# Kernel optimization log

Measured on AMD Instinct MI355X. Metric: run time of the kernel, lower is better.

The kernel has to match this reference:

```python
import jax, jax.numpy as jnp
import numpy as np

C = 256
CK = C // 8  # query/key projection dim

def conv1x1(x, w, b):
    # x: (B,C,H,W), w: (O,C), b: (O,)
    return jnp.einsum('bchw,oc->bohw', x, w) + b[None, :, None, None]

def conv3x3(x, w, b):
    # w: (O,C,3,3)
    y = jax.lax.conv_general_dilated(x, w, window_strides=(1, 1), padding='SAME',
                                     dimension_numbers=('NCHW', 'OIHW', 'NCHW'))
    return y + b[None, :, None, None]

def setup_inputs() -> dict:
    key = jax.random.key(0)
    ks = jax.random.split(key, 24)
    s = 0.05
    d = {
        'x1': jax.random.normal(ks[0], (4, C, 64, 64), jnp.float32),
        'x2': jax.random.normal(ks[1], (4, C, 64, 64), jnp.float32),
        'wq1': jax.random.normal(ks[2], (CK, C), jnp.float32) * s,
        'bq1': jax.random.normal(ks[3], (CK,), jnp.float32) * s,
        'wk1': jax.random.normal(ks[4], (CK, C), jnp.float32) * s,
        'bk1': jax.random.normal(ks[5], (CK,), jnp.float32) * s,
        'wv1': jax.random.normal(ks[6], (C, C), jnp.float32) * s,
        'bv1': jax.random.normal(ks[7], (C,), jnp.float32) * s,
        'wq2': jax.random.normal(ks[8], (CK, C), jnp.float32) * s,
        'bq2': jax.random.normal(ks[9], (CK,), jnp.float32) * s,
        'wk2': jax.random.normal(ks[10], (CK, C), jnp.float32) * s,
        'bk2': jax.random.normal(ks[11], (CK,), jnp.float32) * s,
        'wv2': jax.random.normal(ks[12], (C, C), jnp.float32) * s,
        'bv2': jax.random.normal(ks[13], (C,), jnp.float32) * s,
        'wd1': jax.random.normal(ks[14], (C, C), jnp.float32) * s,
        'bd1': jax.random.normal(ks[15], (C,), jnp.float32) * s,
        'wd3': jax.random.normal(ks[16], (C, C, 3, 3), jnp.float32) * s,
        'bd3': jax.random.normal(ks[17], (C,), jnp.float32) * s,
        'gamma1': jax.random.normal(ks[18], (1,), jnp.float32) * 0.5,
        'gamma2': jax.random.normal(ks[19], (1,), jnp.float32) * 0.5,
    }
    return d

def reference(x1, x2, wq1, bq1, wk1, bk1, wv1, bv1, wq2, bq2, wk2, bk2, wv2, bv2,
              wd1, bd1, wd3, bd3, gamma1, gamma2):
    B, Cc, H, W = x1.shape
    N = H * W
    # projections (1x1 convs), flattened to (B, d, N)
    q1 = conv1x1(x1, wq1, bq1).reshape(B, CK, N)
    k1 = conv1x1(x1, wk1, bk1).reshape(B, CK, N)
    v1 = conv1x1(x1, wv1, bv1).reshape(B, Cc, N)
    q2 = conv1x1(x2, wq2, bq2).reshape(B, CK, N)
    k2 = conv1x1(x2, wk2, bk2).reshape(B, CK, N)
    v2 = conv1x1(x2, wv2, bv2).reshape(B, Cc, N)
    # cross attention 1: queries from x1, keys/values from x2
    energy1 = jnp.einsum('bdi,bdj->bij', q1, k2)          # (B,N,N)
    attn1 = jax.nn.softmax(energy1, axis=-1)
    out1 = jnp.einsum('bcj,bij->bci', v2, attn1).reshape(B, Cc, H, W)
    # cross attention 2: queries from x2, keys/values from x1
    energy2 = jnp.einsum('bdi,bdj->bij', q2, k1)
    attn2 = jax.nn.softmax(energy2, axis=-1)
    out2 = jnp.einsum('bcj,bij->bci', v1, attn2).reshape(B, Cc, H, W)
    # residual conv branches + gamma-scaled skip (norm1/norm2 in source are dead code)
    out1 = out1 + conv1x1(x1, wd1, bd1) + conv3x3(x1, wd3, bd3)
    out2 = out2 + conv1x1(x2, wd1, bd1) + conv3x3(x2, wd3, bd3)
    out1 = x1 + gamma1[0] * out1
    out2 = x2 + gamma2[0] * out2
    return (out1, out2)
```

## Files before the change

kernel.cpp:

```cpp
#include <hip/hip_runtime.h>
#include <hip/hip_bf16.h>

#define CC 256
#define CKD 32
#define NN 4096
#define HH 64
#define WW 64
#define BB 4

#define LOG2E 1.44269504088896f
#define EXPSHIFT 23.0831203874f

typedef __attribute__((ext_vector_type(8))) short short8;
typedef __attribute__((ext_vector_type(4))) float floatx4;

__device__ __forceinline__ unsigned f2bf(float f) {
  union { float f; unsigned u; } v; v.f = f;
  unsigned r = v.u + 0x7fffu + ((v.u >> 16) & 1u);
  return r >> 16;
}
__device__ __forceinline__ unsigned f2bf_fast(float f) {
  return (__float_as_uint(f) + 0x8000u) >> 16;
}
__device__ __forceinline__ float fast_exp2(float x) {
#if __has_builtin(__builtin_amdgcn_exp2f)
  return __builtin_amdgcn_exp2f(x);
#else
  return __expf(x * 0.693147181f);
#endif
}
__device__ __forceinline__ float bf_lo(unsigned u) { return __uint_as_float(u << 16); }
__device__ __forceinline__ float bf_hi(unsigned u) { return __uint_as_float(u & 0xffff0000u); }

__device__ __forceinline__ void bar_lds() {
  asm volatile("s_waitcnt lgkmcnt(0)" ::: "memory");
  __builtin_amdgcn_s_barrier();
}

__global__ __launch_bounds__(256) void xpack_kernel(
    const float* __restrict__ x1, const float* __restrict__ x2,
    unsigned short* __restrict__ Xp) {
  const int t = threadIdx.x;
  const int nb = blockIdx.x, cbk = blockIdx.y, img = blockIdx.z;
  const float* X = ((img >> 2) ? x2 : x1) + (size_t)(img & 3) * CC * NN;
  const int n0 = nb * 64, c0 = cbk * 64;
  __shared__ float tile[64][65];
  const int nl = t & 63, cl0 = t >> 6;
#pragma unroll
  for (int i = 0; i < 16; ++i)
    tile[cl0 + i * 4][nl] = X[(size_t)(c0 + cl0 + i * 4) * NN + n0 + nl];
  __syncthreads();
#pragma unroll
  for (int it = 0; it < 2; ++it) {
    int id = it * 256 + t;
    int nl2 = id >> 3, cc = id & 7;
    short8 v;
#pragma unroll
    for (int j = 0; j < 8; ++j) v[j] = (short)f2bf(tile[cc * 8 + j][nl2]);
    *(short8*)(Xp + (size_t)img * NN * CC + (size_t)(n0 + nl2) * CC + c0 + cc * 8) = v;
  }
}

__global__ __launch_bounds__(256) void wpack_kernel(
    const float* __restrict__ wd1, const float* __restrict__ wd3,
    const float* __restrict__ wq1, const float* __restrict__ wk1,
    const float* __restrict__ wv1,
    const float* __restrict__ wq2, const float* __restrict__ wk2,
    const float* __restrict__ wv2,
    const float* __restrict__ bq1, const float* __restrict__ bk1,
    const float* __restrict__ bv1,
    const float* __restrict__ bq2, const float* __restrict__ bk2,
    const float* __restrict__ bv2,
    unsigned short* __restrict__ Wp, unsigned short* __restrict__ Wqkv,
    float* __restrict__ Bias) {
  const int id = blockIdx.x * 256 + threadIdx.x;
#pragma unroll
  for (int tap = 0; tap < 10; ++tap) {
    float v = (tap < 9) ? wd3[(size_t)id * 9 + tap] : wd1[id];
    Wp[(size_t)tap * (CC * CC) + id] = (unsigned short)f2bf(v);
  }
#pragma unroll
  for (int j = 0; j < 3; ++j) {
    int e = id + j * 65536;
    if (e < 2 * 320 * 256) {
      int inp = e / (320 * 256), rem = e % (320 * 256);
      int o = rem >> 8, c = rem & 255;
      float v;
      if (inp == 0)
        v = (o < 32) ? wq1[o * 256 + c] * LOG2E
            : (o < 64) ? wk1[(o - 32) * 256 + c] : wv1[(o - 64) * 256 + c];
      else
        v = (o < 32) ? wq2[o * 256 + c] * LOG2E
            : (o < 64) ? wk2[(o - 32) * 256 + c] : wv2[(o - 64) * 256 + c];
      Wqkv[e] = (unsigned short)f2bf(v);
    }
  }
  if (id < 640) {
    int inp = id / 320, o = id % 320;
    float v;
    if (inp == 0) v = (o < 32) ? bq1[o] * LOG2E
                      : (o < 64) ? bk1[o - 32] : bv1[o - 64];
    else          v = (o < 32) ? bq2[o] * LOG2E
                      : (o < 64) ? bk2[o - 32] : bv2[o - 64];
    Bias[id] = v;
  }
}

__global__ __launch_bounds__(256) void proj_mfma_kernel(
    const unsigned short* __restrict__ Xp, const unsigned short* __restrict__ Wqkv,
    const float* __restrict__ Bias,
    unsigned short* __restrict__ Qp1, unsigned short* __restrict__ Kp1,
    unsigned short* __restrict__ Vp1,
    unsigned short* __restrict__ Qp2, unsigned short* __restrict__ Kp2,
    unsigned short* __restrict__ Vp2) {
  const int t = threadIdx.x;
  const int w = t >> 6, lane = t & 63;
  const int l15 = lane & 15, g = lane >> 4;
  const int img = blockIdx.x, pb = blockIdx.y;
  const int pix0 = pb * 64;
  const int inp = img >> 2, b = img & 3;
  const unsigned short* Xi = Xp + (size_t)img * NN * CC;
  const unsigned short* Wb = Wqkv + (size_t)inp * 320 * CC;
  const float* Bi = Bias + inp * 320;
  unsigned short* Qp = (inp ? Qp2 : Qp1) + (size_t)b * NN * CKD;
  unsigned short* Kp = (inp ? Kp2 : Kp1) + (size_t)b * NN * CKD;
  unsigned short* Vp = (inp ? Vp2 : Vp1) + (size_t)b * NN * CC;

  __shared__ unsigned short tile[320][72];

  floatx4 acc[4][5];
#pragma unroll
  for (int mf = 0; mf < 4; ++mf)
#pragma unroll
    for (int nf = 0; nf < 5; ++nf) acc[mf][nf] = (floatx4){0.f, 0.f, 0.f, 0.f};
  const int o0w = w * 80;

#pragma unroll
  for (int cb = 0; cb < 8; ++cb) {
    short8 a[4], bfr[5];
#pragma unroll
    for (int mf = 0; mf < 4; ++mf)
      a[mf] = *(const short8*)(Xi + (size_t)(pix0 + mf * 16 + l15) * CC + cb * 32 + g * 8);
#pragma unroll
    for (int nf = 0; nf < 5; ++nf)
      bfr[nf] = *(const short8*)(Wb + (size_t)(o0w + nf * 16 + l15) * CC + cb * 32 + g * 8);
#pragma unroll
    for (int nf = 0; nf < 5; ++nf)
#pragma unroll
      for (int mf = 0; mf < 4; ++mf)
        acc[mf][nf] = __builtin_amdgcn_mfma_f32_16x16x32_bf16(
            a[mf], bfr[nf], acc[mf][nf], 0, 0, 0);
  }

#pragma unroll
  for (int nf = 0; nf < 5; ++nf) {
    float bs = Bi[o0w + nf * 16 + l15];
#pragma unroll
    for (int mf = 0; mf < 4; ++mf) {
      uint2 pk;
      pk.x = f2bf(acc[mf][nf][0] + bs) | (f2bf(acc[mf][nf][1] + bs) << 16);
      pk.y = f2bf(acc[mf][nf][2] + bs) | (f2bf(acc[mf][nf][3] + bs) << 16);
      *(uint2*)&tile[o0w + nf * 16 + l15][mf * 16 + g * 4] = pk;
    }
  }
  __syncthreads();

  {
    const int pix = t >> 2, ch = t & 3;
    short8 vq, vk;
#pragma unroll
    for (int e = 0; e < 8; ++e) {
      vq[e] = (short)tile[ch * 8 + e][pix];
      vk[e] = (short)tile[32 + ch * 8 + e][pix];
    }
    *(short8*)(Qp + (size_t)(pix0 + pix) * CKD + ch * 8) = vq;
    *(short8*)(Kp + (size_t)(pix0 + pix) * CKD + ch * 8) = vk;
  }
#pragma unroll
  for (int it = 0; it < 8; ++it) {
    short8 vv = *(const short8*)&tile[64 + t][it * 8];
    *(short8*)(Vp + ((size_t)((pix0 >> 3) + it) * CC + t) * 8) = vv;
  }
}

__global__ __launch_bounds__(256, 2) void attn_kernel(
    const unsigned short* __restrict__ Qp1, const unsigned short* __restrict__ Kp1,
    const unsigned short* __restrict__ Qp2, const unsigned short* __restrict__ Kp2,
    const unsigned short* __restrict__ Vp1, const unsigned short* __restrict__ Vp2,
    const unsigned short* __restrict__ Xp, const unsigned short* __restrict__ Wp,
    const float* __restrict__ bd1, const float* __restrict__ bd3,
    const float* __restrict__ x1, const float* __restrict__ x2,
    const float* __restrict__ g1, const float* __restrict__ g2,
    float* __restrict__ out) {
  const int t = threadIdx.x;
  const int w = t >> 6, lane = t & 63;
  const int l15 = lane & 15, g = lane >> 4;
  const int att = blockIdx.x, b = blockIdx.y;
  const int yblk = blockIdx.z;
  const int i0 = yblk * 64;

  const unsigned short *Qp, *Kp, *Vp; const float *x; float gamma; float* o;
  if (att == 0) { Qp = Qp1; Kp = Kp2; Vp = Vp2; x = x1; gamma = g1[0]; o = out; }
  else          { Qp = Qp2; Kp = Kp1; Vp = Vp1; x = x2; gamma = g2[0];
                  o = out + (size_t)BB * CC * NN; }
  Qp += (size_t)b * NN * CKD; Kp += (size_t)b * NN * CKD; Vp += (size_t)b * NN * CC;
  x += (size_t)b * CC * NN; o += (size_t)b * CC * NN;
  const unsigned short* Xi = Xp + (size_t)(att * 4 + b) * NN * CC;

  __shared__ union {
    unsigned short xs[3][66][72];
    unsigned short ps[2][64][72];
  } u;
  __shared__ unsigned short cres[256][68];
  __shared__ float l_s[64];

  short8 bq = *(const short8*)(Qp + (size_t)(i0 + w * 16 + l15) * CKD + g * 8);

  floatx4 acc[4][4];
#pragma unroll
  for (int a = 0; a < 4; ++a)
#pragma unroll
    for (int c = 0; c < 4; ++c) acc[a][c] = (floatx4){0.f, 0.f, 0.f, 0.f};
  float l_acc = 0.f;
  const floatx4 zinit = {-EXPSHIFT, -EXPSHIFT, -EXPSHIFT, -EXPSHIFT};

  short8 kr[2][4], vr[2][8];
  auto LOADK = [&](int tt, short8* d) {
    const unsigned short* kb = Kp + ((size_t)tt * 64 + l15) * CKD + g * 8;
#pragma unroll
    for (int js = 0; js < 4; ++js) d[js] = *(const short8*)(kb + js * 16 * CKD);
  };
  auto LOADV = [&](int tt, short8* d) {
#pragma unroll
    for (int ks = 0; ks < 2; ++ks)
#pragma unroll
      for (int cs = 0; cs < 4; ++cs)
        d[ks * 4 + cs] = *(const short8*)(Vp +
            (((size_t)tt * 8 + ks * 4 + g) * CC + (w * 64 + cs * 16 + l15)) * 8);
  };
  auto GEMM1 = [&](const short8* kb, unsigned short (*ps)[72]) {
#pragma unroll
    for (int js = 0; js < 4; ++js) {
      floatx4 s = __builtin_amdgcn_mfma_f32_16x16x32_bf16(kb[js], bq, zinit, 0, 0, 0);
      float p0 = fast_exp2(s[0]);
      float p1 = fast_exp2(s[1]);
      float p2 = fast_exp2(s[2]);
      float p3 = fast_exp2(s[3]);
      l_acc += (p0 + p1) + (p2 + p3);
      unsigned u0 = __float_as_uint(p0) + 0x8000u;
      unsigned u1 = __float_as_uint(p1) + 0x8000u;
      unsigned u2 = __float_as_uint(p2) + 0x8000u;
      unsigned u3 = __float_as_uint(p3) + 0x8000u;
      uint2 pk;
      pk.x = __builtin_amdgcn_perm(u1, u0, 0x07060302u);
      pk.y = __builtin_amdgcn_perm(u3, u2, 0x07060302u);
      *(uint2*)&ps[w * 16 + l15][js * 16 + g * 4] = pk;
    }
  };
  auto GEMM2 = [&](const short8* vb, unsigned short (*ps)[72]) {
#pragma unroll
    for (int ks = 0; ks < 2; ++ks) {
      short8 ap[4];
#pragma unroll
      for (int isub = 0; isub < 4; ++isub)
        ap[isub] = *(const short8*)&ps[isub * 16 + l15][ks * 32 + g * 8];
#pragma unroll
      for (int cs = 0; cs < 4; ++cs)
#pragma unroll
        for (int isub = 0; isub < 4; ++isub)
          acc[isub][cs] = __builtin_amdgcn_mfma_f32_16x16x32_bf16(
              ap[isub], vb[ks * 4 + cs], acc[isub][cs], 0, 0, 0);
    }
  };

  LOADK(0, kr[0]); LOADK(1, kr[1]); LOADV(0, vr[0]);

  {
    floatx4 ac[4][4];
#pragma unroll
    for (int pm = 0; pm < 4; ++pm)
#pragma unroll
      for (int on = 0; on < 4; ++on) ac[pm][on] = (floatx4){0.f, 0.f, 0.f, 0.f};

    for (int cb = 0; cb < 4; ++cb) {
      const int c0 = cb * 64;
      if (cb) bar_lds();
#pragma unroll
      for (int it = 0; it < 7; ++it) {
        int id = it * 256 + t;
        if (id < 1584) {
          int r = id / 528, rem = id % 528;
          int col = rem >> 3, cc = rem & 7;
          int y = yblk - 1 + r, xx = col - 1;
          short8 v = {0, 0, 0, 0, 0, 0, 0, 0};
          if (y >= 0 && y < HH && xx >= 0 && xx < WW)
            v = *(const short8*)(Xi + (size_t)(y * WW + xx) * CC + c0 + cc * 8);
          *(short8*)&u.xs[r][col][cc * 8] = v;
        }
      }
      bar_lds();
#pragma unroll
      for (int tap = 0; tap < 10; ++tap) {
        const int dy = (tap < 9) ? tap / 3 - 1 : 0;
        const int dx = (tap < 9) ? tap % 3 - 1 : 0;
        const unsigned short* wrow =
            Wp + ((size_t)tap * CC + w * 64 + l15) * CC + c0 + g * 8;
#pragma unroll
        for (int ks = 0; ks < 2; ++ks) {
          short8 af[4], bw[4];
#pragma unroll
          for (int pm = 0; pm < 4; ++pm)
            af[pm] = *(const short8*)&u.xs[1 + dy][1 + pm * 16 + l15 + dx][ks * 32 + g * 8];
#pragma unroll
          for (int on = 0; on < 4; ++on)
            bw[on] = *(const short8*)(wrow + (size_t)(on * 16) * CC + ks * 32);
#pragma unroll
          for (int pm = 0; pm < 4; ++pm)
#pragma unroll
            for (int on = 0; on < 4; ++on)
              ac[pm][on] = __builtin_amdgcn_mfma_f32_16x16x32_bf16(
                  af[pm], bw[on], ac[pm][on], 0, 0, 0);
        }
      }
    }
#pragma unroll
    for (int on = 0; on < 4; ++on) {
      int oo = w * 64 + on * 16 + l15;
      float bs = bd1[oo] + bd3[oo];
#pragma unroll
      for (int pm = 0; pm < 4; ++pm) {
        uint2 pk;
        pk.x = f2bf_fast(ac[pm][on][0] + bs) | (f2bf_fast(ac[pm][on][1] + bs) << 16);
        pk.y = f2bf_fast(ac[pm][on][2] + bs) | (f2bf_fast(ac[pm][on][3] + bs) << 16);
        *(uint2*)&cres[oo][pm * 16 + g * 4] = pk;
      }
    }
  }
  bar_lds();

  GEMM1(kr[0], u.ps[0]);
  bar_lds();

  for (int jt = 0; jt < 64; jt += 2) {
    if (jt + 2 < 64) LOADK(jt + 2, kr[0]);
    LOADV(jt + 1, vr[1]);
    GEMM1(kr[1], u.ps[1]);
    GEMM2(vr[0], u.ps[0]);
    bar_lds();
    if (jt + 3 < 64) LOADK(jt + 3, kr[1]);
    if (jt + 2 < 64) { LOADV(jt + 2, vr[0]); GEMM1(kr[0], u.ps[0]); }
    GEMM2(vr[1], u.ps[1]);
    bar_lds();
  }

  l_acc += __shfl_xor(l_acc, 16);
  l_acc += __shfl_xor(l_acc, 32);
  if (g == 0) l_s[w * 16 + l15] = l_acc;
  bar_lds();

#pragma unroll
  for (int isub = 0; isub < 4; ++isub) {
    float linv[4];
#pragma unroll
    for (int r = 0; r < 4; ++r) linv[r] = 1.f / l_s[isub * 16 + g * 4 + r];
#pragma unroll
    for (int cs = 0; cs < 4; ++cs) {
      int c = w * 64 + cs * 16 + l15;
      size_t base = (size_t)c * NN + i0 + isub * 16 + g * 4;
      float4 xr = *(const float4*)(x + base);
      uint2 cr = *(const uint2*)&cres[c][isub * 16 + g * 4];
      float4 ov;
      ov.x = xr.x + gamma * (acc[isub][cs][0] * linv[0] + bf_lo(cr.x));
      ov.y = xr.y + gamma * (acc[isub][cs][1] * linv[1] + bf_hi(cr.x));
      ov.z = xr.z + gamma * (acc[isub][cs][2] * linv[2] + bf_lo(cr.y));
      ov.w = xr.w + gamma * (acc[isub][cs][3] * linv[3] + bf_hi(cr.y));
      *(float4*)(o + base) = ov;
    }
  }
}

extern "C" void kernel_launch(void* const* d_in, const int* in_sizes, int n_in,
                              void* d_out, int out_size, void* d_ws, size_t ws_size,
                              hipStream_t stream) {
  const float* x1  = (const float*)d_in[0];
  const float* x2  = (const float*)d_in[1];
  const float* wq1 = (const float*)d_in[2];
  const float* bq1 = (const float*)d_in[3];
  const float* wk1 = (const float*)d_in[4];
  const float* bk1 = (const float*)d_in[5];
  const float* wv1 = (const float*)d_in[6];
  const float* bv1 = (const float*)d_in[7];
  const float* wq2 = (const float*)d_in[8];
  const float* bq2 = (const float*)d_in[9];
  const float* wk2 = (const float*)d_in[10];
  const float* bk2 = (const float*)d_in[11];
  const float* wv2 = (const float*)d_in[12];
  const float* bv2 = (const float*)d_in[13];
  const float* wd1 = (const float*)d_in[14];
  const float* bd1 = (const float*)d_in[15];
  const float* wd3 = (const float*)d_in[16];
  const float* bd3 = (const float*)d_in[17];
  const float* g1  = (const float*)d_in[18];
  const float* g2  = (const float*)d_in[19];
  float* out = (float*)d_out;

  const size_t QB = (size_t)BB * NN * CKD * 2;
  const size_t VB = (size_t)BB * NN * CC * 2;
  const size_t XB = (size_t)2 * BB * NN * CC * 2;
  const size_t WPB = (size_t)10 * CC * CC * 2;
  const size_t WQB = (size_t)2 * 320 * CC * 2;
  char* base = (char*)d_ws;
  unsigned short* Qp1 = (unsigned short*)(base);
  unsigned short* Kp1 = (unsigned short*)(base + QB);
  unsigned short* Qp2 = (unsigned short*)(base + 2 * QB);
  unsigned short* Kp2 = (unsigned short*)(base + 3 * QB);
  unsigned short* Vp1 = (unsigned short*)(base + 4 * QB);
  unsigned short* Vp2 = (unsigned short*)(base + 4 * QB + VB);
  unsigned short* Xp  = (unsigned short*)(base + 4 * QB + 2 * VB);
  unsigned short* Wp  = (unsigned short*)(base + 4 * QB + 2 * VB + XB);
  unsigned short* Wqkv = (unsigned short*)(base + 4 * QB + 2 * VB + XB + WPB);
  float* Bias = (float*)(base + 4 * QB + 2 * VB + XB + WPB + WQB);

  xpack_kernel<<<dim3(NN / 64, CC / 64, 2 * BB), 256, 0, stream>>>(x1, x2, Xp);
  wpack_kernel<<<dim3(CC * CC / 256), 256, 0, stream>>>(
      wd1, wd3, wq1, wk1, wv1, wq2, wk2, wv2,
      bq1, bk1, bv1, bq2, bk2, bv2, Wp, Wqkv, Bias);

  proj_mfma_kernel<<<dim3(2 * BB, NN / 64), 256, 0, stream>>>(
      Xp, Wqkv, Bias, Qp1, Kp1, Vp1, Qp2, Kp2, Vp2);

  attn_kernel<<<dim3(2, BB, NN / 64), 256, 0, stream>>>(
      Qp1, Kp1, Qp2, Kp2, Vp1, Vp2, Xp, Wp, bd1, bd3, x1, x2, g1, g2, out);
}
```

Measured before the change: 302.1 us.

## Load conv3x3 input tiles directly from global memory and raise occupancy to 3 blocks

Removes the LDS staging of the 3-row input halo for the fused 3x3/1x1 conv. Each MFMA operand fragment is now read straight from global memory with bounds-checked zero padding, which also removes the per-channel-block barriers. The smaller LDS footprint (no union, narrower cres padding) plus launch_bounds 3 are meant to fit more blocks per CU. In exchange there are many redundant, uncoalesced global loads that rely on L1/L2 hits, register pressure is tighter, and the cres row stride of 66 may cause LDS bank conflicts.

```diff
diff --git a/kernel.cpp b/kernel.cpp
--- a/kernel.cpp
+++ b/kernel.cpp
@@ -183,7 +183,7 @@
   }
 }
 
-__global__ __launch_bounds__(256, 2) void attn_kernel(
+__global__ __launch_bounds__(256, 3) void attn_kernel(
     const unsigned short* __restrict__ Qp1, const unsigned short* __restrict__ Kp1,
     const unsigned short* __restrict__ Qp2, const unsigned short* __restrict__ Kp2,
     const unsigned short* __restrict__ Vp1, const unsigned short* __restrict__ Vp2,
@@ -207,11 +207,8 @@
   x += (size_t)b * CC * NN; o += (size_t)b * CC * NN;
   const unsigned short* Xi = Xp + (size_t)(att * 4 + b) * NN * CC;
 
-  __shared__ union {
-    unsigned short xs[3][66][72];
-    unsigned short ps[2][64][72];
-  } u;
-  __shared__ unsigned short cres[256][68];
+  __shared__ unsigned short ps[2][64][72];
+  __shared__ unsigned short cres[256][66];
   __shared__ float l_s[64];
 
   short8 bq = *(const short8*)(Qp + (size_t)(i0 + w * 16 + l15) * CKD + g * 8);
@@ -238,7 +235,7 @@
         d[ks * 4 + cs] = *(const short8*)(Vp +
             (((size_t)tt * 8 + ks * 4 + g) * CC + (w * 64 + cs * 16 + l15)) * 8);
   };
-  auto GEMM1 = [&](const short8* kb, unsigned short (*ps)[72]) {
+  auto GEMM1 = [&](const short8* kb, unsigned short (*psb)[72]) {
 #pragma unroll
     for (int js = 0; js < 4; ++js) {
       floatx4 s = __builtin_amdgcn_mfma_f32_16x16x32_bf16(kb[js], bq, zinit, 0, 0, 0);
@@ -254,16 +251,16 @@
       uint2 pk;
       pk.x = __builtin_amdgcn_perm(u1, u0, 0x07060302u);
       pk.y = __builtin_amdgcn_perm(u3, u2, 0x07060302u);
-      *(uint2*)&ps[w * 16 + l15][js * 16 + g * 4] = pk;
+      *(uint2*)&psb[w * 16 + l15][js * 16 + g * 4] = pk;
     }
   };
-  auto GEMM2 = [&](const short8* vb, unsigned short (*ps)[72]) {
+  auto GEMM2 = [&](const short8* vb, unsigned short (*psb)[72]) {
 #pragma unroll
     for (int ks = 0; ks < 2; ++ks) {
       short8 ap[4];
 #pragma unroll
       for (int isub = 0; isub < 4; ++isub)
-        ap[isub] = *(const short8*)&ps[isub * 16 + l15][ks * 32 + g * 8];
+        ap[isub] = *(const short8*)&psb[isub * 16 + l15][ks * 32 + g * 8];
 #pragma unroll
       for (int cs = 0; cs < 4; ++cs)
 #pragma unroll
@@ -284,33 +281,24 @@
 
     for (int cb = 0; cb < 4; ++cb) {
       const int c0 = cb * 64;
-      if (cb) bar_lds();
-#pragma unroll
-      for (int it = 0; it < 7; ++it) {
-        int id = it * 256 + t;
-        if (id < 1584) {
-          int r = id / 528, rem = id % 528;
-          int col = rem >> 3, cc = rem & 7;
-          int y = yblk - 1 + r, xx = col - 1;
-          short8 v = {0, 0, 0, 0, 0, 0, 0, 0};
-          if (y >= 0 && y < HH && xx >= 0 && xx < WW)
-            v = *(const short8*)(Xi + (size_t)(y * WW + xx) * CC + c0 + cc * 8);
-          *(short8*)&u.xs[r][col][cc * 8] = v;
-        }
-      }
-      bar_lds();
 #pragma unroll
       for (int tap = 0; tap < 10; ++tap) {
         const int dy = (tap < 9) ? tap / 3 - 1 : 0;
         const int dx = (tap < 9) ? tap % 3 - 1 : 0;
+        const int y = yblk + dy;
         const unsigned short* wrow =
             Wp + ((size_t)tap * CC + w * 64 + l15) * CC + c0 + g * 8;
 #pragma unroll
         for (int ks = 0; ks < 2; ++ks) {
           short8 af[4], bw[4];
 #pragma unroll
-          for (int pm = 0; pm < 4; ++pm)
-            af[pm] = *(const short8*)&u.xs[1 + dy][1 + pm * 16 + l15 + dx][ks * 32 + g * 8];
+          for (int pm = 0; pm < 4; ++pm) {
+            const int px = pm * 16 + l15 + dx;
+            short8 v = {0, 0, 0, 0, 0, 0, 0, 0};
+            if (((unsigned)y < (unsigned)HH) & ((unsigned)px < (unsigned)WW))
+              v = *(const short8*)(Xi + (size_t)(y * WW + px) * CC + c0 + ks * 32 + g * 8);
+            af[pm] = v;
+          }
 #pragma unroll
           for (int on = 0; on < 4; ++on)
             bw[on] = *(const short8*)(wrow + (size_t)(on * 16) * CC + ks * 32);
@@ -336,20 +324,19 @@
       }
     }
   }
-  bar_lds();
-
-  GEMM1(kr[0], u.ps[0]);
+
+  GEMM1(kr[0], ps[0]);
   bar_lds();
 
   for (int jt = 0; jt < 64; jt += 2) {
     if (jt + 2 < 64) LOADK(jt + 2, kr[0]);
     LOADV(jt + 1, vr[1]);
-    GEMM1(kr[1], u.ps[1]);
-    GEMM2(vr[0], u.ps[0]);
+    GEMM1(kr[1], ps[1]);
+    GEMM2(vr[0], ps[0]);
     bar_lds();
     if (jt + 3 < 64) LOADK(jt + 3, kr[1]);
-    if (jt + 2 < 64) { LOADV(jt + 2, vr[0]); GEMM1(kr[0], u.ps[0]); }
-    GEMM2(vr[1], u.ps[1]);
+    if (jt + 2 < 64) { LOADV(jt + 2, vr[0]); GEMM1(kr[0], ps[0]); }
+    GEMM2(vr[1], ps[1]);
     bar_lds();
   }
 
```

Result: slower. 527.7 us (+74.6%).

## Split attention blocks across channel halves and fold conv into attention accumulators

Applied to the files above, without the earlier changes.

The attention kernel now launches twice as many blocks, each handling half of the output channels. Each warp covers 32 query rows by 64 channels, which halves the accumulator registers and lets occupancy rise to 4 blocks per CU. The residual conv is now computed after attention, accumulating straight into the normalized attention accumulators, so the bf16 cres LDS buffer and its rounding go away. The cost is that GEMM1 (QK^T plus exp) is computed twice, once in each channel-half block, and the K/V pipeline is reworked to single-step double buffering.

```diff
diff --git a/kernel.cpp b/kernel.cpp
--- a/kernel.cpp
+++ b/kernel.cpp
@@ -18,9 +18,6 @@
   union { float f; unsigned u; } v; v.f = f;
   unsigned r = v.u + 0x7fffu + ((v.u >> 16) & 1u);
   return r >> 16;
-}
-__device__ __forceinline__ unsigned f2bf_fast(float f) {
-  return (__float_as_uint(f) + 0x8000u) >> 16;
 }
 __device__ __forceinline__ float fast_exp2(float x) {
 #if __has_builtin(__builtin_amdgcn_exp2f)
@@ -183,7 +180,7 @@
   }
 }
 
-__global__ __launch_bounds__(256, 2) void attn_kernel(
+__global__ __launch_bounds__(256, 4) void attn_kernel(
     const unsigned short* __restrict__ Qp1, const unsigned short* __restrict__ Kp1,
     const unsigned short* __restrict__ Qp2, const unsigned short* __restrict__ Kp2,
     const unsigned short* __restrict__ Vp1, const unsigned short* __restrict__ Vp2,
@@ -195,9 +192,12 @@
   const int t = threadIdx.x;
   const int w = t >> 6, lane = t & 63;
   const int l15 = lane & 15, g = lane >> 4;
-  const int att = blockIdx.x, b = blockIdx.y;
+  const int att = blockIdx.x >> 1, chh = blockIdx.x & 1;
+  const int b = blockIdx.y;
   const int yblk = blockIdx.z;
   const int i0 = yblk * 64;
+  const int ip = w & 1, cq = w >> 1;
+  const int ch0 = chh * 128 + cq * 64;
 
   const unsigned short *Qp, *Kp, *Vp; const float *x; float gamma; float* o;
   if (att == 0) { Qp = Qp1; Kp = Kp2; Vp = Vp2; x = x1; gamma = g1[0]; o = out; }
@@ -208,40 +208,37 @@
   const unsigned short* Xi = Xp + (size_t)(att * 4 + b) * NN * CC;
 
   __shared__ union {
+    unsigned short ps[2][64][72];
     unsigned short xs[3][66][72];
-    unsigned short ps[2][64][72];
   } u;
-  __shared__ unsigned short cres[256][68];
   __shared__ float l_s[64];
 
   short8 bq = *(const short8*)(Qp + (size_t)(i0 + w * 16 + l15) * CKD + g * 8);
 
-  floatx4 acc[4][4];
-#pragma unroll
-  for (int a = 0; a < 4; ++a)
-#pragma unroll
-    for (int c = 0; c < 4; ++c) acc[a][c] = (floatx4){0.f, 0.f, 0.f, 0.f};
+  floatx4 acc[2][4];
+#pragma unroll
+  for (int is = 0; is < 2; ++is)
+#pragma unroll
+    for (int c = 0; c < 4; ++c) acc[is][c] = (floatx4){0.f, 0.f, 0.f, 0.f};
   float l_acc = 0.f;
   const floatx4 zinit = {-EXPSHIFT, -EXPSHIFT, -EXPSHIFT, -EXPSHIFT};
 
-  short8 kr[2][4], vr[2][8];
-  auto LOADK = [&](int tt, short8* d) {
+  short8 kr[4], vA[4], vB[4];
+  auto LOADK = [&](int tt) {
     const unsigned short* kb = Kp + ((size_t)tt * 64 + l15) * CKD + g * 8;
 #pragma unroll
-    for (int js = 0; js < 4; ++js) d[js] = *(const short8*)(kb + js * 16 * CKD);
+    for (int js = 0; js < 4; ++js) kr[js] = *(const short8*)(kb + js * 16 * CKD);
   };
-  auto LOADV = [&](int tt, short8* d) {
-#pragma unroll
-    for (int ks = 0; ks < 2; ++ks)
-#pragma unroll
-      for (int cs = 0; cs < 4; ++cs)
-        d[ks * 4 + cs] = *(const short8*)(Vp +
-            (((size_t)tt * 8 + ks * 4 + g) * CC + (w * 64 + cs * 16 + l15)) * 8);
+  auto LOADVH = [&](int tt, int ks, short8* d) {
+#pragma unroll
+    for (int cs = 0; cs < 4; ++cs)
+      d[cs] = *(const short8*)(Vp +
+          (((size_t)tt * 8 + ks * 4 + g) * CC + (ch0 + cs * 16 + l15)) * 8);
   };
-  auto GEMM1 = [&](const short8* kb, unsigned short (*ps)[72]) {
+  auto GEMM1 = [&](unsigned short (*psb)[72]) {
 #pragma unroll
     for (int js = 0; js < 4; ++js) {
-      floatx4 s = __builtin_amdgcn_mfma_f32_16x16x32_bf16(kb[js], bq, zinit, 0, 0, 0);
+      floatx4 s = __builtin_amdgcn_mfma_f32_16x16x32_bf16(kr[js], bq, zinit, 0, 0, 0);
       float p0 = fast_exp2(s[0]);
       float p1 = fast_exp2(s[1]);
       float p2 = fast_exp2(s[2]);
@@ -254,104 +251,40 @@
       uint2 pk;
       pk.x = __builtin_amdgcn_perm(u1, u0, 0x07060302u);
       pk.y = __builtin_amdgcn_perm(u3, u2, 0x07060302u);
-      *(uint2*)&ps[w * 16 + l15][js * 16 + g * 4] = pk;
+      *(uint2*)&psb[w * 16 + l15][js * 16 + g * 4] = pk;
     }
   };
-  auto GEMM2 = [&](const short8* vb, unsigned short (*ps)[72]) {
-#pragma unroll
-    for (int ks = 0; ks < 2; ++ks) {
-      short8 ap[4];
-#pragma unroll
-      for (int isub = 0; isub < 4; ++isub)
-        ap[isub] = *(const short8*)&ps[isub * 16 + l15][ks * 32 + g * 8];
-#pragma unroll
-      for (int cs = 0; cs < 4; ++cs)
-#pragma unroll
-        for (int isub = 0; isub < 4; ++isub)
-          acc[isub][cs] = __builtin_amdgcn_mfma_f32_16x16x32_bf16(
-              ap[isub], vb[ks * 4 + cs], acc[isub][cs], 0, 0, 0);
-    }
+  auto GEMM2ks = [&](int ks, const short8* vb, unsigned short (*psb)[72]) {
+    short8 ap[2];
+#pragma unroll
+    for (int is = 0; is < 2; ++is)
+      ap[is] = *(const short8*)&psb[(ip * 2 + is) * 16 + l15][ks * 32 + g * 8];
+#pragma unroll
+    for (int cs = 0; cs < 4; ++cs)
+#pragma unroll
+      for (int is = 0; is < 2; ++is)
+        acc[is][cs] = __builtin_amdgcn_mfma_f32_16x16x32_bf16(
+            ap[is], vb[cs], acc[is][cs], 0, 0, 0);
   };
 
-  LOADK(0, kr[0]); LOADK(1, kr[1]); LOADV(0, vr[0]);
-
-  {
-    floatx4 ac[4][4];
-#pragma unroll
-    for (int pm = 0; pm < 4; ++pm)
-#pragma unroll
-      for (int on = 0; on < 4; ++on) ac[pm][on] = (floatx4){0.f, 0.f, 0.f, 0.f};
-
-    for (int cb = 0; cb < 4; ++cb) {
-      const int c0 = cb * 64;
-      if (cb) bar_lds();
-#pragma unroll
-      for (int it = 0; it < 7; ++it) {
-        int id = it * 256 + t;
-        if (id < 1584) {
-          int r = id / 528, rem = id % 528;
-          int col = rem >> 3, cc = rem & 7;
-          int y = yblk - 1 + r, xx = col - 1;
-          short8 v = {0, 0, 0, 0, 0, 0, 0, 0};
-          if (y >= 0 && y < HH && xx >= 0 && xx < WW)
-            v = *(const short8*)(Xi + (size_t)(y * WW + xx) * CC + c0 + cc * 8);
-          *(short8*)&u.xs[r][col][cc * 8] = v;
-        }
-      }
-      bar_lds();
-#pragma unroll
-      for (int tap = 0; tap < 10; ++tap) {
-        const int dy = (tap < 9) ? tap / 3 - 1 : 0;
-        const int dx = (tap < 9) ? tap % 3 - 1 : 0;
-        const unsigned short* wrow =
-            Wp + ((size_t)tap * CC + w * 64 + l15) * CC + c0 + g * 8;
-#pragma unroll
-        for (int ks = 0; ks < 2; ++ks) {
-          short8 af[4], bw[4];
-#pragma unroll
-          for (int pm = 0; pm < 4; ++pm)
-            af[pm] = *(const short8*)&u.xs[1 + dy][1 + pm * 16 + l15 + dx][ks * 32 + g * 8];
-#pragma unroll
-          for (int on = 0; on < 4; ++on)
-            bw[on] = *(const short8*)(wrow + (size_t)(on * 16) * CC + ks * 32);
-#pragma unroll
-          for (int pm = 0; pm < 4; ++pm)
-#pragma unroll
-            for (int on = 0; on < 4; ++on)
-              ac[pm][on] = __builtin_amdgcn_mfma_f32_16x16x32_bf16(
-                  af[pm], bw[on], ac[pm][on], 0, 0, 0);
-        }
-      }
-    }
-#pragma unroll
-    for (int on = 0; on < 4; ++on) {
-      int oo = w * 64 + on * 16 + l15;
-      float bs = bd1[oo] + bd3[oo];
-#pragma unroll
-      for (int pm = 0; pm < 4; ++pm) {
-        uint2 pk;
-        pk.x = f2bf_fast(ac[pm][on][0] + bs) | (f2bf_fast(ac[pm][on][1] + bs) << 16);
-        pk.y = f2bf_fast(ac[pm][on][2] + bs) | (f2bf_fast(ac[pm][on][3] + bs) << 16);
-        *(uint2*)&cres[oo][pm * 16 + g * 4] = pk;
-      }
-    }
-  }
+  LOADK(0); LOADVH(0, 0, vA); LOADVH(0, 1, vB);
+  GEMM1(u.ps[0]);
+  LOADK(1);
   bar_lds();
 
-  GEMM1(kr[0], u.ps[0]);
-  bar_lds();
-
-  for (int jt = 0; jt < 64; jt += 2) {
-    if (jt + 2 < 64) LOADK(jt + 2, kr[0]);
-    LOADV(jt + 1, vr[1]);
-    GEMM1(kr[1], u.ps[1]);
-    GEMM2(vr[0], u.ps[0]);
+  for (int jt = 0; jt < 63; ++jt) {
+    unsigned short (*pcur)[72] = u.ps[jt & 1];
+    unsigned short (*pnxt)[72] = u.ps[(jt & 1) ^ 1];
+    GEMM1(pnxt);
+    if (jt < 62) LOADK(jt + 2);
+    GEMM2ks(0, vA, pcur);
+    LOADVH(jt + 1, 0, vA);
+    GEMM2ks(1, vB, pcur);
+    LOADVH(jt + 1, 1, vB);
     bar_lds();
-    if (jt + 3 < 64) LOADK(jt + 3, kr[1]);
-    if (jt + 2 < 64) { LOADV(jt + 2, vr[0]); GEMM1(kr[0], u.ps[0]); }
-    GEMM2(vr[1], u.ps[1]);
-    bar_lds();
-  }
+  }
+  GEMM2ks(0, vA, u.ps[1]);
+  GEMM2ks(1, vB, u.ps[1]);
 
   l_acc += __shfl_xor(l_acc, 16);
   l_acc += __shfl_xor(l_acc, 32);
@@ -359,21 +292,73 @@
   bar_lds();
 
 #pragma unroll
-  for (int isub = 0; isub < 4; ++isub) {
+  for (int is = 0; is < 2; ++is) {
     float linv[4];
 #pragma unroll
-    for (int r = 0; r < 4; ++r) linv[r] = 1.f / l_s[isub * 16 + g * 4 + r];
+    for (int r = 0; r < 4; ++r)
+      linv[r] = 1.f / l_s[ip * 32 + is * 16 + g * 4 + r];
+#pragma unroll
+    for (int cs = 0; cs < 4; ++cs)
+#pragma unroll
+      for (int r = 0; r < 4; ++r) acc[is][cs][r] *= linv[r];
+  }
+
+  for (int cb = 0; cb < 4; ++cb) {
+    const int c0 = cb * 64;
+    bar_lds();
+#pragma unroll
+    for (int it = 0; it < 7; ++it) {
+      int id = it * 256 + t;
+      if (id < 1584) {
+        int r = id / 528, rem = id % 528;
+        int col = rem >> 3, cc = rem & 7;
+        int y = yblk - 1 + r, xx = col - 1;
+        short8 v = {0, 0, 0, 0, 0, 0, 0, 0};
+        if (y >= 0 && y < HH && xx >= 0 && xx < WW)
+          v = *(const short8*)(Xi + (size_t)(y * WW + xx) * CC + c0 + cc * 8);
+        *(short8*)&u.xs[r][col][cc * 8] = v;
+      }
+    }
+    bar_lds();
+#pragma unroll
+    for (int tap = 0; tap < 10; ++tap) {
+      const int dy = (tap < 9) ? tap / 3 - 1 : 0;
+      const int dx = (tap < 9) ? tap % 3 - 1 : 0;
+      const unsigned short* wrow =
+          Wp + ((size_t)tap * CC + ch0 + l15) * CC + c0 + g * 8;
+#pragma unroll
+      for (int ks = 0; ks < 2; ++ks) {
+        short8 af[2], bw[4];
+#pragma unroll
+        for (int is = 0; is < 2; ++is)
+          af[is] = *(const short8*)
+              &u.xs[1 + dy][1 + ip * 32 + is * 16 + l15 + dx][ks * 32 + g * 8];
+#pragma unroll
+        for (int cs = 0; cs < 4; ++cs)
+          bw[cs] = *(const short8*)(wrow + (size_t)(cs * 16) * CC + ks * 32);
+#pragma unroll
+        for (int is = 0; is < 2; ++is)
+#pragma unroll
+          for (int cs = 0; cs < 4; ++cs)
+            acc[is][cs] = __builtin_amdgcn_mfma_f32_16x16x32_bf16(
+                af[is], bw[cs], acc[is][cs], 0, 0, 0);
+      }
+    }
+  }
+
+#pragma unroll
+  for (int is = 0; is < 2; ++is) {
 #pragma unroll
     for (int cs = 0; cs < 4; ++cs) {
-      int c = w * 64 + cs * 16 + l15;
-      size_t base = (size_t)c * NN + i0 + isub * 16 + g * 4;
+      int c = ch0 + cs * 16 + l15;
+      float bs = bd1[c] + bd3[c];
+      size_t base = (size_t)c * NN + i0 + ip * 32 + is * 16 + g * 4;
       float4 xr = *(const float4*)(x + base);
-      uint2 cr = *(const uint2*)&cres[c][isub * 16 + g * 4];
       float4 ov;
-      ov.x = xr.x + gamma * (acc[isub][cs][0] * linv[0] + bf_lo(cr.x));
-      ov.y = xr.y + gamma * (acc[isub][cs][1] * linv[1] + bf_hi(cr.x));
-      ov.z = xr.z + gamma * (acc[isub][cs][2] * linv[2] + bf_lo(cr.y));
-      ov.w = xr.w + gamma * (acc[isub][cs][3] * linv[3] + bf_hi(cr.y));
+      ov.x = xr.x + gamma * (acc[is][cs][0] + bs);
+      ov.y = xr.y + gamma * (acc[is][cs][1] + bs);
+      ov.z = xr.z + gamma * (acc[is][cs][2] + bs);
+      ov.w = xr.w + gamma * (acc[is][cs][3] + bs);
       *(float4*)(o + base) = ov;
     }
   }
@@ -429,6 +414,6 @@
   proj_mfma_kernel<<<dim3(2 * BB, NN / 64), 256, 0, stream>>>(
       Xp, Wqkv, Bias, Qp1, Kp1, Vp1, Qp2, Kp2, Vp2);
 
-  attn_kernel<<<dim3(2, BB, NN / 64), 256, 0, stream>>>(
+  attn_kernel<<<dim3(4, BB, NN / 64), 256, 0, stream>>>(
       Qp1, Kp1, Qp2, Kp2, Vp1, Vp2, Xp, Wp, bd1, bd3, x1, x2, g1, g2, out);
 }
```

After: 414.8 us. +37.3%, slower.

## Run conv after attention into shared accumulator, deepen P buffer ring

Applied to the files above, without the earlier changes.

The fused conv branch now runs after the attention loop. It accumulates directly into the attention accumulators once those have been normalised by the softmax sum, which removes the separate conv accumulator set and the bf16 cres staging buffer in LDS. The P tile buffer grows from 2 to 4 slots, so the attention loop needs only one barrier per pair of key tiles, and K/V loads are issued further ahead. This lowers register and LDS pressure and synchronisation, but the LDS union is now larger (ps is 4x64x72) and the conv input loads are no longer overlapped with the K/V prefetch.

```diff
diff --git a/kernel.cpp b/kernel.cpp
--- a/kernel.cpp
+++ b/kernel.cpp
@@ -18,9 +18,6 @@
   union { float f; unsigned u; } v; v.f = f;
   unsigned r = v.u + 0x7fffu + ((v.u >> 16) & 1u);
   return r >> 16;
-}
-__device__ __forceinline__ unsigned f2bf_fast(float f) {
-  return (__float_as_uint(f) + 0x8000u) >> 16;
 }
 __device__ __forceinline__ float fast_exp2(float x) {
 #if __has_builtin(__builtin_amdgcn_exp2f)
@@ -208,10 +205,9 @@
   const unsigned short* Xi = Xp + (size_t)(att * 4 + b) * NN * CC;
 
   __shared__ union {
+    unsigned short ps[4][64][72];
     unsigned short xs[3][66][72];
-    unsigned short ps[2][64][72];
   } u;
-  __shared__ unsigned short cres[256][68];
   __shared__ float l_s[64];
 
   short8 bq = *(const short8*)(Qp + (size_t)(i0 + w * 16 + l15) * CKD + g * 8);
@@ -238,7 +234,7 @@
         d[ks * 4 + cs] = *(const short8*)(Vp +
             (((size_t)tt * 8 + ks * 4 + g) * CC + (w * 64 + cs * 16 + l15)) * 8);
   };
-  auto GEMM1 = [&](const short8* kb, unsigned short (*ps)[72]) {
+  auto GEMM1 = [&](const short8* kb, unsigned short (*psb)[72]) {
 #pragma unroll
     for (int js = 0; js < 4; ++js) {
       floatx4 s = __builtin_amdgcn_mfma_f32_16x16x32_bf16(kb[js], bq, zinit, 0, 0, 0);
@@ -254,16 +250,16 @@
       uint2 pk;
       pk.x = __builtin_amdgcn_perm(u1, u0, 0x07060302u);
       pk.y = __builtin_amdgcn_perm(u3, u2, 0x07060302u);
-      *(uint2*)&ps[w * 16 + l15][js * 16 + g * 4] = pk;
+      *(uint2*)&psb[w * 16 + l15][js * 16 + g * 4] = pk;
     }
   };
-  auto GEMM2 = [&](const short8* vb, unsigned short (*ps)[72]) {
+  auto GEMM2 = [&](const short8* vb, unsigned short (*psb)[72]) {
 #pragma unroll
     for (int ks = 0; ks < 2; ++ks) {
       short8 ap[4];
 #pragma unroll
       for (int isub = 0; isub < 4; ++isub)
-        ap[isub] = *(const short8*)&ps[isub * 16 + l15][ks * 32 + g * 8];
+        ap[isub] = *(const short8*)&psb[isub * 16 + l15][ks * 32 + g * 8];
 #pragma unroll
       for (int cs = 0; cs < 4; ++cs)
 #pragma unroll
@@ -273,84 +269,27 @@
     }
   };
 
-  LOADK(0, kr[0]); LOADK(1, kr[1]); LOADV(0, vr[0]);
-
-  {
-    floatx4 ac[4][4];
-#pragma unroll
-    for (int pm = 0; pm < 4; ++pm)
-#pragma unroll
-      for (int on = 0; on < 4; ++on) ac[pm][on] = (floatx4){0.f, 0.f, 0.f, 0.f};
-
-    for (int cb = 0; cb < 4; ++cb) {
-      const int c0 = cb * 64;
-      if (cb) bar_lds();
-#pragma unroll
-      for (int it = 0; it < 7; ++it) {
-        int id = it * 256 + t;
-        if (id < 1584) {
-          int r = id / 528, rem = id % 528;
-          int col = rem >> 3, cc = rem & 7;
-          int y = yblk - 1 + r, xx = col - 1;
-          short8 v = {0, 0, 0, 0, 0, 0, 0, 0};
-          if (y >= 0 && y < HH && xx >= 0 && xx < WW)
-            v = *(const short8*)(Xi + (size_t)(y * WW + xx) * CC + c0 + cc * 8);
-          *(short8*)&u.xs[r][col][cc * 8] = v;
-        }
-      }
-      bar_lds();
-#pragma unroll
-      for (int tap = 0; tap < 10; ++tap) {
-        const int dy = (tap < 9) ? tap / 3 - 1 : 0;
-        const int dx = (tap < 9) ? tap % 3 - 1 : 0;
-        const unsigned short* wrow =
-            Wp + ((size_t)tap * CC + w * 64 + l15) * CC + c0 + g * 8;
-#pragma unroll
-        for (int ks = 0; ks < 2; ++ks) {
-          short8 af[4], bw[4];
-#pragma unroll
-          for (int pm = 0; pm < 4; ++pm)
-            af[pm] = *(const short8*)&u.xs[1 + dy][1 + pm * 16 + l15 + dx][ks * 32 + g * 8];
-#pragma unroll
-          for (int on = 0; on < 4; ++on)
-            bw[on] = *(const short8*)(wrow + (size_t)(on * 16) * CC + ks * 32);
-#pragma unroll
-          for (int pm = 0; pm < 4; ++pm)
-#pragma unroll
-            for (int on = 0; on < 4; ++on)
-              ac[pm][on] = __builtin_amdgcn_mfma_f32_16x16x32_bf16(
-                  af[pm], bw[on], ac[pm][on], 0, 0, 0);
-        }
-      }
-    }
-#pragma unroll
-    for (int on = 0; on < 4; ++on) {
-      int oo = w * 64 + on * 16 + l15;
-      float bs = bd1[oo] + bd3[oo];
-#pragma unroll
-      for (int pm = 0; pm < 4; ++pm) {
-        uint2 pk;
-        pk.x = f2bf_fast(ac[pm][on][0] + bs) | (f2bf_fast(ac[pm][on][1] + bs) << 16);
-        pk.y = f2bf_fast(ac[pm][on][2] + bs) | (f2bf_fast(ac[pm][on][3] + bs) << 16);
-        *(uint2*)&cres[oo][pm * 16 + g * 4] = pk;
-      }
-    }
-  }
+  LOADK(0, kr[0]); LOADK(1, kr[1]);
+  LOADV(0, vr[0]); LOADV(1, vr[1]);
+  GEMM1(kr[0], u.ps[0]);
+  GEMM1(kr[1], u.ps[1]);
+  LOADK(2, kr[0]); LOADK(3, kr[1]);
   bar_lds();
 
-  GEMM1(kr[0], u.ps[0]);
-  bar_lds();
-
   for (int jt = 0; jt < 64; jt += 2) {
-    if (jt + 2 < 64) LOADK(jt + 2, kr[0]);
-    LOADV(jt + 1, vr[1]);
-    GEMM1(kr[1], u.ps[1]);
-    GEMM2(vr[0], u.ps[0]);
-    bar_lds();
-    if (jt + 3 < 64) LOADK(jt + 3, kr[1]);
-    if (jt + 2 < 64) { LOADV(jt + 2, vr[0]); GEMM1(kr[0], u.ps[0]); }
-    GEMM2(vr[1], u.ps[1]);
-    bar_lds();
+    if (jt + 2 < 64) {
+      GEMM1(kr[0], u.ps[(jt + 2) & 3]);
+      if (jt + 4 < 64) LOADK(jt + 4, kr[0]);
+    }
+    GEMM2(vr[0], u.ps[jt & 3]);
+    if (jt + 2 < 64) LOADV(jt + 2, vr[0]);
+    if (jt + 3 < 64) {
+      GEMM1(kr[1], u.ps[(jt + 3) & 3]);
+      if (jt + 5 < 64) LOADK(jt + 5, kr[1]);
+    }
+    GEMM2(vr[1], u.ps[(jt + 1) & 3]);
+    if (jt + 3 < 64) LOADV(jt + 3, vr[1]);
+    if (jt + 2 < 64) bar_lds();
   }
 
   l_acc += __shfl_xor(l_acc, 16);
@@ -364,16 +303,66 @@
 #pragma unroll
     for (int r = 0; r < 4; ++r) linv[r] = 1.f / l_s[isub * 16 + g * 4 + r];
 #pragma unroll
+    for (int cs = 0; cs < 4; ++cs)
+#pragma unroll
+      for (int r = 0; r < 4; ++r) acc[isub][cs][r] *= linv[r];
+  }
+
+  for (int cb = 0; cb < 4; ++cb) {
+    const int c0 = cb * 64;
+    if (cb) bar_lds();
+#pragma unroll
+    for (int it = 0; it < 7; ++it) {
+      int id = it * 256 + t;
+      if (id < 1584) {
+        int r = id / 528, rem = id % 528;
+        int col = rem >> 3, cc = rem & 7;
+        int y = yblk - 1 + r, xx = col - 1;
+        short8 v = {0, 0, 0, 0, 0, 0, 0, 0};
+        if (y >= 0 && y < HH && xx >= 0 && xx < WW)
+          v = *(const short8*)(Xi + (size_t)(y * WW + xx) * CC + c0 + cc * 8);
+        *(short8*)&u.xs[r][col][cc * 8] = v;
+      }
+    }
+    bar_lds();
+#pragma unroll
+    for (int tap = 0; tap < 10; ++tap) {
+      const int dy = (tap < 9) ? tap / 3 - 1 : 0;
+      const int dx = (tap < 9) ? tap % 3 - 1 : 0;
+      const unsigned short* wrow =
+          Wp + ((size_t)tap * CC + w * 64 + l15) * CC + c0 + g * 8;
+#pragma unroll
+      for (int ks = 0; ks < 2; ++ks) {
+        short8 af[4], bw[4];
+#pragma unroll
+        for (int pm = 0; pm < 4; ++pm)
+          af[pm] = *(const short8*)&u.xs[1 + dy][1 + pm * 16 + l15 + dx][ks * 32 + g * 8];
+#pragma unroll
+        for (int on = 0; on < 4; ++on)
+          bw[on] = *(const short8*)(wrow + (size_t)(on * 16) * CC + ks * 32);
+#pragma unroll
+        for (int pm = 0; pm < 4; ++pm)
+#pragma unroll
+          for (int on = 0; on < 4; ++on)
+            acc[pm][on] = __builtin_amdgcn_mfma_f32_16x16x32_bf16(
+                af[pm], bw[on], acc[pm][on], 0, 0, 0);
+      }
+    }
+  }
+
+#pragma unroll
+  for (int isub = 0; isub < 4; ++isub) {
+#pragma unroll
     for (int cs = 0; cs < 4; ++cs) {
       int c = w * 64 + cs * 16 + l15;
+      float bs = bd1[c] + bd3[c];
       size_t base = (size_t)c * NN + i0 + isub * 16 + g * 4;
       float4 xr = *(const float4*)(x + base);
-      uint2 cr = *(const uint2*)&cres[c][isub * 16 + g * 4];
       float4 ov;
-      ov.x = xr.x + gamma * (acc[isub][cs][0] * linv[0] + bf_lo(cr.x));
-      ov.y = xr.y + gamma * (acc[isub][cs][1] * linv[1] + bf_hi(cr.x));
-      ov.z = xr.z + gamma * (acc[isub][cs][2] * linv[2] + bf_lo(cr.y));
-      ov.w = xr.w + gamma * (acc[isub][cs][3] * linv[3] + bf_hi(cr.y));
+      ov.x = xr.x + gamma * (acc[isub][cs][0] + bs);
+      ov.y = xr.y + gamma * (acc[isub][cs][1] + bs);
+      ov.z = xr.z + gamma * (acc[isub][cs][2] + bs);
+      ov.w = xr.w + gamma * (acc[isub][cs][3] + bs);
       *(float4*)(o + base) = ov;
     }
   }
```

Result: no change. 296.8 us (-1.8%).
